# Kernel optimization log

Hardware: AMD Instinct MI355X
Metric: run time of the kernel (lower is better)

The kernel has to match this reference:

```python
import jax, jax.numpy as jnp
import numpy as np

GROUP = 128  # W4A16 quantization group size along the input (reduction) dim


def dequant(q, s, z):
    """Dequantize int4 weights. q: [out, in] ints in [0,16); s, z: [out, in//GROUP]."""
    out_f, in_f = q.shape
    g = in_f // GROUP
    qf = q.reshape(out_f, g, GROUP).astype(s.dtype)
    w = (qf - z[:, :, None]) * s[:, :, None]
    return w.reshape(out_f, in_f)


def setup_inputs() -> dict:
    key = jax.random.key(0)
    ks = jax.random.split(key, 11)
    H, I = 4096, 11008
    B, S = 4, 2048
    x = jax.random.normal(ks[0], (B, S, H), dtype=jnp.float32)
    qw_gate = jax.random.randint(ks[1], (I, H), 0, 16, dtype=jnp.int32)
    qw_up = jax.random.randint(ks[2], (I, H), 0, 16, dtype=jnp.int32)
    qw_down = jax.random.randint(ks[3], (H, I), 0, 16, dtype=jnp.int32)
    # scales small so dequantized weights have realistic magnitude; zeros in [0,16)
    s_gate = jax.random.uniform(ks[4], (I, H // GROUP), dtype=jnp.float32) * 0.01
    z_gate = jax.random.uniform(ks[5], (I, H // GROUP), dtype=jnp.float32) * 16.0
    s_up = jax.random.uniform(ks[6], (I, H // GROUP), dtype=jnp.float32) * 0.01
    z_up = jax.random.uniform(ks[7], (I, H // GROUP), dtype=jnp.float32) * 16.0
    s_down = jax.random.uniform(ks[8], (H, I // GROUP), dtype=jnp.float32) * 0.01
    z_down = jax.random.uniform(ks[9], (H, I // GROUP), dtype=jnp.float32) * 16.0
    return {
        "x": x,
        "qw_gate": qw_gate, "qw_up": qw_up, "qw_down": qw_down,
        "s_gate": s_gate, "z_gate": z_gate,
        "s_up": s_up, "z_up": z_up,
        "s_down": s_down, "z_down": z_down,
    }


def reference(x, qw_gate, qw_up, qw_down, s_gate, z_gate, s_up, z_up, s_down, z_down):
    # W4A16 SwiGLU MLP: down( silu(gate(x)) * up(x) )
    Wg = dequant(qw_gate, s_gate, z_gate)   # [I, H]
    Wu = dequant(qw_up, s_up, z_up)         # [I, H]
    Wd = dequant(qw_down, s_down, z_down)   # [H, I]
    g = jnp.einsum('bsh,ih->bsi', x, Wg)
    u = jnp.einsum('bsh,ih->bsi', x, Wu)
    h = jax.nn.silu(g) * u
    return jnp.einsum('bsi,hi->bsh', h, Wd)
```

## Files before the change

kernel.cpp:

```cpp
#include <hip/hip_runtime.h>
#include <hip/hip_fp16.h>

typedef __attribute__((ext_vector_type(8))) short s16x8;
typedef __attribute__((ext_vector_type(8))) _Float16 f16x8;
typedef __attribute__((ext_vector_type(4))) float f32x4;

__global__ void cvt_f32_to_f16_kernel(const float* __restrict__ in,
                                      __half* __restrict__ out, long n) {
  long i = (long)blockIdx.x * blockDim.x + threadIdx.x;
  long stride = (long)gridDim.x * blockDim.x;
  const float4* p4 = (const float4*)in;
  for (long j = i; j * 8 < n; j += stride) {
    float4 a = p4[j * 2];
    float4 b = p4[j * 2 + 1];
    union { s16x8 v; __half2 h2[4]; } w;
    w.h2[0] = __floats2half2_rn(a.x, a.y);
    w.h2[1] = __floats2half2_rn(a.z, a.w);
    w.h2[2] = __floats2half2_rn(b.x, b.y);
    w.h2[3] = __floats2half2_rn(b.z, b.w);
    *(s16x8*)(out + j * 8) = w.v;
  }
}

__global__ void pack_kernel(const int* __restrict__ q, uint32_t* __restrict__ p,
                            long n8) {
  long i = (long)blockIdx.x * blockDim.x + threadIdx.x;
  long stride = (long)gridDim.x * blockDim.x;
  for (; i < n8; i += stride) {
    int4 a = ((const int4*)q)[2 * i];
    int4 b = ((const int4*)q)[2 * i + 1];
    uint32_t w = (uint32_t)a.x | ((uint32_t)a.y << 4) | ((uint32_t)a.z << 8) |
                 ((uint32_t)a.w << 12) | ((uint32_t)b.x << 16) |
                 ((uint32_t)b.y << 20) | ((uint32_t)b.z << 24) |
                 ((uint32_t)b.w << 28);
    p[i] = w;
  }
}

__device__ __forceinline__ s16x8 dq_compute(int4 q0, int4 q1, float s, float z) {
  __half hs = __float2half(s);
  __half2 s2 = __halves2half2(hs, hs);
  __half hc = __float2half(-(64.f + z) * s);
  __half2 c2 = __halves2half2(hc, hc);
  uint32_t b0 = 0x54005400u + ((uint32_t)q0.x << 4) + ((uint32_t)q0.y << 20);
  uint32_t b1 = 0x54005400u + ((uint32_t)q0.z << 4) + ((uint32_t)q0.w << 20);
  uint32_t b2 = 0x54005400u + ((uint32_t)q1.x << 4) + ((uint32_t)q1.y << 20);
  uint32_t b3 = 0x54005400u + ((uint32_t)q1.z << 4) + ((uint32_t)q1.w << 20);
  union { s16x8 v; __half2 h2[4]; } w;
  w.h2[0] = __hfma2(*(__half2*)&b0, s2, c2);
  w.h2[1] = __hfma2(*(__half2*)&b1, s2, c2);
  w.h2[2] = __hfma2(*(__half2*)&b2, s2, c2);
  w.h2[3] = __hfma2(*(__half2*)&b3, s2, c2);
  return w.v;
}

__device__ __forceinline__ s16x8 dq8(uint32_t w, __half2 s2, __half2 c2) {
  union { s16x8 v; __half2 h2[4]; } r;
#pragma unroll
  for (int i = 0; i < 4; ++i) {
    uint32_t t = (w >> (8 * i)) & 0xFFu;
    uint32_t b = 0x54005400u + ((t & 15u) << 4) + ((t >> 4) << 20);
    r.h2[i] = __hfma2(*(__half2*)&b, s2, c2);
  }
  return r.v;
}

__device__ __forceinline__ int xcd_swz(int w0, int nwg) {
  const int q = nwg >> 3, r = nwg & 7;
  const int xcd = w0 & 7, idx = w0 >> 3;
  const int base = (xcd < r) ? xcd * (q + 1) : r * (q + 1) + (xcd - r) * q;
  return base + idx;
}

template <int EPI, int PK>
__global__ __launch_bounds__(512, 2)
void qgemm_x_kernel(const __half* __restrict__ Xh,
                    const int* __restrict__ Q, const uint32_t* __restrict__ QP,
                    const float* __restrict__ S, const float* __restrict__ Z,
                    __half* __restrict__ Pan, int mbs) {
  constexpr int H = 4096, I = 11008, G = 32;
  const int wg = xcd_swz(blockIdx.x, gridDim.x);
  const int mb = wg % mbs;
  const int nb = wg / mbs;
  const int m0 = mb * 256;
  const int n0 = nb * 128;
  const int tid = threadIdx.x;
  const int lane = tid & 63;
  const int wave = tid >> 6;
  const int wm = (wave >> 1) * 64, wn = (wave & 1) * 64;
  const int l15 = lane & 15, lq = lane >> 4;
  const int rsw = (l15 & 7) << 3;

  __shared__ __half As[2][256][64];
  __shared__ __half Bs[2][128][64];

  f32x4 acc[4][4];
#pragma unroll
  for (int i = 0; i < 4; ++i)
#pragma unroll
    for (int j = 0; j < 4; ++j) acc[i][j] = {0.f, 0.f, 0.f, 0.f};

  const int arowD = tid >> 3;
  const int acolD = (((tid & 7) ^ ((tid >> 3) & 7)) << 3);
  const int qrow = tid >> 2, qcol0 = (tid & 3) * 16, qsw = (qrow & 7) << 3;
  const int*      qP  = Q  + (size_t)(n0 + qrow) * H + qcol0;
  const uint32_t* qPp = QP + (size_t)(n0 + qrow) * (H / 8) + (tid & 3) * 2;
  const float* sP = S + (size_t)(n0 + qrow) * G;
  const float* zP = Z + (size_t)(n0 + qrow) * G;

  int4 qA[4], qB[4];
  uint32_t wA0, wA1, wB0, wB1;
  float sA, zA, sB, zB;

#define STAGE_A(buf, kk)                                              \
  {                                                                   \
    const int _k = (kk);                                              \
    _Pragma("unroll")                                                 \
    for (int c = 0; c < 4; ++c) {                                     \
      const __half* src = Xh + (size_t)(m0 + c * 64 + arowD) * H + _k + acolD; \
      __half* dst = &As[buf][0][0] + (size_t)(c * 512 + tid) * 8;     \
      __builtin_amdgcn_global_load_lds((const __attribute__((address_space(1))) void*)src, \
                                       (__attribute__((address_space(3))) void*)dst, 16, 0, 0); \
    }                                                                 \
  }
#define LOAD_Q(set, kk)                                               \
  {                                                                   \
    const int _k = (kk);                                              \
    if (PK) {                                                         \
      w##set##0 = qPp[_k >> 3]; w##set##1 = qPp[(_k >> 3) + 1];       \
    } else {                                                          \
      _Pragma("unroll")                                               \
      for (int i = 0; i < 4; ++i) q##set[i] = ((const int4*)(qP + _k))[i]; \
    }                                                                 \
    s##set = sP[_k >> 7]; z##set = zP[_k >> 7];                       \
  }
#define WRITE_B(buf, set)                                             \
  {                                                                   \
    if (PK) {                                                         \
      __half hs = __float2half(s##set);                               \
      __half2 s2 = __halves2half2(hs, hs);                            \
      __half hc = __float2half(-(64.f + z##set) * s##set);            \
      __half2 c2 = __halves2half2(hc, hc);                            \
      *(s16x8*)&Bs[buf][qrow][(qcol0 + 0) ^ qsw] = dq8(w##set##0, s2, c2); \
      *(s16x8*)&Bs[buf][qrow][(qcol0 + 8) ^ qsw] = dq8(w##set##1, s2, c2); \
    } else {                                                          \
      *(s16x8*)&Bs[buf][qrow][(qcol0 + 0) ^ qsw] = dq_compute(q##set[0], q##set[1], s##set, z##set); \
      *(s16x8*)&Bs[buf][qrow][(qcol0 + 8) ^ qsw] = dq_compute(q##set[2], q##set[3], s##set, z##set); \
    }                                                                 \
  }
#define MFMA_BUF(buf)                                                 \
  {                                                                   \
    __builtin_amdgcn_s_setprio(1);                                    \
    _Pragma("unroll")                                                 \
    for (int kk = 0; kk < 2; ++kk) {                                  \
      const int cbase = (kk * 32 + lq * 8) ^ rsw;                     \
      f16x8 af[4];                                                    \
      _Pragma("unroll")                                               \
      for (int i = 0; i < 4; ++i)                                     \
        af[i] = *(const f16x8*)&As[buf][wm + i * 16 + l15][cbase];    \
      _Pragma("unroll")                                               \
      for (int j = 0; j < 4; ++j) {                                   \
        f16x8 bf = *(const f16x8*)&Bs[buf][wn + j * 16 + l15][cbase]; \
        _Pragma("unroll")                                             \
        for (int i = 0; i < 4; ++i)                                   \
          acc[i][j] = __builtin_amdgcn_mfma_f32_16x16x32_f16(af[i], bf, acc[i][j], 0, 0, 0); \
      }                                                               \
    }                                                                 \
    __builtin_amdgcn_s_setprio(0);                                    \
  }

  const int nt = H / 64;
  STAGE_A(0, 0)
  LOAD_Q(A, 0)
  LOAD_Q(B, 64)
  WRITE_B(0, A)
  __syncthreads();

  for (int t = 0; t < nt; t += 2) {
    if (t + 1 < nt) STAGE_A(1, (t + 1) * 64)
    if (t + 2 < nt) LOAD_Q(A, (t + 2) * 64)
    MFMA_BUF(0)
    if (t + 1 < nt) WRITE_B(1, B)
    __syncthreads();
    if (t + 2 < nt) STAGE_A(0, (t + 2) * 64)
    if (t + 3 < nt) LOAD_Q(B, (t + 3) * 64)
    MFMA_BUF(1)
    if (t + 2 < nt) WRITE_B(0, A)
    __syncthreads();
  }
#undef STAGE_A
#undef LOAD_Q
#undef WRITE_B
#undef MFMA_BUF

#pragma unroll
  for (int i = 0; i < 4; ++i)
#pragma unroll
    for (int j = 0; j < 4; ++j)
#pragma unroll
      for (int r = 0; r < 4; ++r) {
        const int row = m0 + wm + i * 16 + lq * 4 + r;
        const int col = n0 + wn + j * 16 + l15;
        const size_t idx = (size_t)row * I + col;
        if (EPI == 0) {
          Pan[idx] = __float2half(acc[i][j][r]);
        } else {
          float g = __half2float(Pan[idx]);
          float u = acc[i][j][r];
          Pan[idx] = __float2half((g / (1.f + __expf(-g))) * u);
        }
      }
}

template <int PK>
__global__ __launch_bounds__(512, 2)
void down_kernel(const __half* __restrict__ Hws,
                 const int* __restrict__ Qd, const uint32_t* __restrict__ QdP,
                 const float* __restrict__ Sd, const float* __restrict__ Zd,
                 float* __restrict__ Out, int mbs) {
  constexpr int K = 11008, N = 4096, G = 86;
  const int wg = xcd_swz(blockIdx.x, gridDim.x);
  const int mb = wg % mbs;
  const int nb = wg / mbs;
  const int m0 = mb * 256, n0 = nb * 128;
  const int tid = threadIdx.x;
  const int lane = tid & 63;
  const int wave = tid >> 6;
  const int wm = (wave >> 1) * 64, wn = (wave & 1) * 64;
  const int l15 = lane & 15, lq = lane >> 4;
  const int rsw = (l15 & 7) << 3;

  __shared__ __half As[2][256][64];
  __shared__ __half Bs[2][128][64];

  f32x4 acc[4][4];
#pragma unroll
  for (int i = 0; i < 4; ++i)
#pragma unroll
    for (int j = 0; j < 4; ++j) acc[i][j] = {0.f, 0.f, 0.f, 0.f};

  const int arowD = tid >> 3;
  const int acolD = (((tid & 7) ^ ((tid >> 3) & 7)) << 3);
  const int qrow = tid >> 2, qcol0 = (tid & 3) * 16, qsw = (qrow & 7) << 3;
  const int*      qP  = Qd  + (size_t)(n0 + qrow) * K + qcol0;
  const uint32_t* qPp = QdP + (size_t)(n0 + qrow) * (K / 8) + (tid & 3) * 2;
  const float* sP = Sd + (size_t)(n0 + qrow) * G;
  const float* zP = Zd + (size_t)(n0 + qrow) * G;

  int4 qA[4], qB[4];
  uint32_t wA0, wA1, wB0, wB1;
  float sA, zA, sB, zB;

#define STAGE_A(buf, kk)                                              \
  {                                                                   \
    const int _k = (kk);                                              \
    _Pragma("unroll")                                                 \
    for (int c = 0; c < 4; ++c) {                                     \
      const __half* src = Hws + (size_t)(m0 + c * 64 + arowD) * K + _k + acolD; \
      __half* dst = &As[buf][0][0] + (size_t)(c * 512 + tid) * 8;     \
      __builtin_amdgcn_global_load_lds((const __attribute__((address_space(1))) void*)src, \
                                       (__attribute__((address_space(3))) void*)dst, 16, 0, 0); \
    }                                                                 \
  }
#define LOAD_Q(set, kk)                                               \
  {                                                                   \
    const int _k = (kk);                                              \
    if (PK) {                                                         \
      w##set##0 = qPp[_k >> 3]; w##set##1 = qPp[(_k >> 3) + 1];       \
    } else {                                                          \
      _Pragma("unroll")                                               \
      for (int i = 0; i < 4; ++i) q##set[i] = ((const int4*)(qP + _k))[i]; \
    }                                                                 \
    s##set = sP[_k >> 7]; z##set = zP[_k >> 7];                       \
  }
#define WRITE_B(buf, set)                                             \
  {                                                                   \
    if (PK) {                                                         \
      __half hs = __float2half(s##set);                               \
      __half2 s2 = __halves2half2(hs, hs);                            \
      __half hc = __float2half(-(64.f + z##set) * s##set);            \
      __half2 c2 = __halves2half2(hc, hc);                            \
      *(s16x8*)&Bs[buf][qrow][(qcol0 + 0) ^ qsw] = dq8(w##set##0, s2, c2); \
      *(s16x8*)&Bs[buf][qrow][(qcol0 + 8) ^ qsw] = dq8(w##set##1, s2, c2); \
    } else {                                                          \
      *(s16x8*)&Bs[buf][qrow][(qcol0 + 0) ^ qsw] = dq_compute(q##set[0], q##set[1], s##set, z##set); \
      *(s16x8*)&Bs[buf][qrow][(qcol0 + 8) ^ qsw] = dq_compute(q##set[2], q##set[3], s##set, z##set); \
    }                                                                 \
  }
#define MFMA_BUF(buf)                                                 \
  {                                                                   \
    __builtin_amdgcn_s_setprio(1);                                    \
    _Pragma("unroll")                                                 \
    for (int kk = 0; kk < 2; ++kk) {                                  \
      const int cbase = (kk * 32 + lq * 8) ^ rsw;                     \
      f16x8 af[4];                                                    \
      _Pragma("unroll")                                               \
      for (int i = 0; i < 4; ++i)                                     \
        af[i] = *(const f16x8*)&As[buf][wm + i * 16 + l15][cbase];    \
      _Pragma("unroll")                                               \
      for (int j = 0; j < 4; ++j) {                                   \
        f16x8 bf = *(const f16x8*)&Bs[buf][wn + j * 16 + l15][cbase]; \
        _Pragma("unroll")                                             \
        for (int i = 0; i < 4; ++i)                                   \
          acc[i][j] = __builtin_amdgcn_mfma_f32_16x16x32_f16(af[i], bf, acc[i][j], 0, 0, 0); \
      }                                                               \
    }                                                                 \
    __builtin_amdgcn_s_setprio(0);                                    \
  }

  const int nt = K / 64;
  STAGE_A(0, 0)
  LOAD_Q(A, 0)
  LOAD_Q(B, 64)
  WRITE_B(0, A)
  __syncthreads();

  for (int t = 0; t < nt; t += 2) {
    if (t + 1 < nt) STAGE_A(1, (t + 1) * 64)
    if (t + 2 < nt) LOAD_Q(A, (t + 2) * 64)
    MFMA_BUF(0)
    if (t + 1 < nt) WRITE_B(1, B)
    __syncthreads();
    if (t + 2 < nt) STAGE_A(0, (t + 2) * 64)
    if (t + 3 < nt) LOAD_Q(B, (t + 3) * 64)
    MFMA_BUF(1)
    if (t + 2 < nt) WRITE_B(0, A)
    __syncthreads();
  }
#undef STAGE_A
#undef LOAD_Q
#undef WRITE_B
#undef MFMA_BUF

#pragma unroll
  for (int i = 0; i < 4; ++i)
#pragma unroll
    for (int j = 0; j < 4; ++j)
#pragma unroll
      for (int r = 0; r < 4; ++r) {
        const int row = m0 + wm + i * 16 + lq * 4 + r;
        const int col = n0 + wn + j * 16 + l15;
        Out[(size_t)row * N + col] = acc[i][j][r];
      }
}

extern "C" void kernel_launch(void* const* d_in, const int* in_sizes, int n_in,
                              void* d_out, int out_size, void* d_ws, size_t ws_size,
                              hipStream_t stream) {
  const float* x  = (const float*)d_in[0];
  const int* qg   = (const int*)d_in[1];
  const int* qu   = (const int*)d_in[2];
  const int* qd   = (const int*)d_in[3];
  const float* sg = (const float*)d_in[4];
  const float* zg = (const float*)d_in[5];
  const float* su = (const float*)d_in[6];
  const float* zu = (const float*)d_in[7];
  const float* sd = (const float*)d_in[8];
  const float* zd = (const float*)d_in[9];
  float* out = (float*)d_out;

  const int M = 8192, H = 4096, I = 11008;
  const long N8 = (long)I * H / 8;

  const int PD_MAX = 1375, PU_MAX = 2751, PG_MAX = 4127;
  uint32_t* Pd = (uint32_t*)d_out;
  uint32_t* Pu = Pd + N8;
  uint32_t* Pg = Pu + N8;

  pack_kernel<<<2048, 256, 0, stream>>>(qd, Pd, N8);
  pack_kernel<<<2048, 256, 0, stream>>>(qu, Pu, N8);
  pack_kernel<<<2048, 256, 0, stream>>>(qg, Pg, N8);

  const size_t per_row = (size_t)(H + I) * 2;
  long mc = (long)(ws_size / per_row);
  mc &= ~255L;
  if (mc > M) mc = M;
  if (mc < 256) mc = 256;
  const int nch = (int)((M + mc - 1) / mc);
  int base = ((M / nch) / 256) * 256;
  if (base < 256) base = 256;
  int rem = M - base * nch;
  const int nplus = rem > 0 ? rem / 256 : 0;

  __half* wsx = (__half*)d_ws;
  const int McMax = base + (nplus > 0 ? 256 : 0);
  __half* wsh = (__half*)((char*)d_ws + (size_t)McMax * H * 2);

  int mbs_arr[64], mb_arr[64];
  {
    int mb = 0;
    for (int c = 0; c < nch; ++c) {
      int r = base + (c < nplus ? 256 : 0);
      mb_arr[c] = mb;
      mbs_arr[c] = r / 256;
      mb += r;
    }
  }

  int W = M;
  for (int c = nch - 1; c >= 0; --c) {
    const int mbase = mb_arr[c];
    const int mbs = mbs_arr[c];
    const int rows = mbs * 256;
    const bool g_pk = (PG_MAX < W);
    const bool u_pk = (PU_MAX < W);
    const bool d_pk = (PD_MAX < mbase);

    cvt_f32_to_f16_kernel<<<1024, 256, 0, stream>>>(
        x + (size_t)mbase * H, wsx, (long)rows * H);

    if (g_pk)
      qgemm_x_kernel<0, 1><<<mbs * (I / 128), 512, 0, stream>>>(
          wsx, qg, Pg, sg, zg, wsh, mbs);
    else
      qgemm_x_kernel<0, 0><<<mbs * (I / 128), 512, 0, stream>>>(
          wsx, qg, Pg, sg, zg, wsh, mbs);

    if (u_pk)
      qgemm_x_kernel<1, 1><<<mbs * (I / 128), 512, 0, stream>>>(
          wsx, qu, Pu, su, zu, wsh, mbs);
    else
      qgemm_x_kernel<1, 0><<<mbs * (I / 128), 512, 0, stream>>>(
          wsx, qu, Pu, su, zu, wsh, mbs);

    if (d_pk)
      down_kernel<1><<<mbs * (H / 128), 512, 0, stream>>>(
          wsh, qd, Pd, sd, zd, out + (size_t)mbase * H, mbs);
    else
      down_kernel<0><<<mbs * (H / 128), 512, 0, stream>>>(
          wsh, qd, Pd, sd, zd, out + (size_t)mbase * H, mbs);

    W = mbase;
  }
}
```

Measured before the change: 3.750 ms.

## Fuse gate and up projections into one kernel with dual accumulators

The separate gate and up GEMM kernels are merged into one gateup kernel that stages each X tile once and multiplies it against both dequantized weight tiles, keeping two accumulator sets and applying SiLU(g)*u in the epilogue. This removes the second read of the fp16 activations and the write-then-read round trip of the gate result through the workspace. In exchange, register pressure doubles (32 f32x4 accumulators) and LDS use grows, which may cut occupancy below the two-blocks-per-CU target. The packed-weight placement in the output buffer and the pack/no-pack thresholds are reordered to fit the fused layout.

```diff
diff --git a/kernel.cpp b/kernel.cpp
--- a/kernel.cpp
+++ b/kernel.cpp
@@ -72,12 +72,14 @@
   return base + idx;
 }
 
-template <int EPI, int PK>
+template <int PK>
 __global__ __launch_bounds__(512, 2)
-void qgemm_x_kernel(const __half* __restrict__ Xh,
-                    const int* __restrict__ Q, const uint32_t* __restrict__ QP,
-                    const float* __restrict__ S, const float* __restrict__ Z,
-                    __half* __restrict__ Pan, int mbs) {
+void gateup_kernel(const __half* __restrict__ Xh,
+                   const int* __restrict__ Qg, const uint32_t* __restrict__ Pg,
+                   const int* __restrict__ Qu, const uint32_t* __restrict__ Pu,
+                   const float* __restrict__ Sg, const float* __restrict__ Zg,
+                   const float* __restrict__ Su, const float* __restrict__ Zu,
+                   __half* __restrict__ Pan, int mbs) {
   constexpr int H = 4096, I = 11008, G = 32;
   const int wg = xcd_swz(blockIdx.x, gridDim.x);
   const int mb = wg % mbs;
@@ -92,25 +94,33 @@
   const int rsw = (l15 & 7) << 3;
 
   __shared__ __half As[2][256][64];
-  __shared__ __half Bs[2][128][64];
-
-  f32x4 acc[4][4];
+  __shared__ __half Bg[2][128][64];
+  __shared__ __half Bu[2][128][64];
+
+  f32x4 accg[4][4], accu[4][4];
 #pragma unroll
   for (int i = 0; i < 4; ++i)
 #pragma unroll
-    for (int j = 0; j < 4; ++j) acc[i][j] = {0.f, 0.f, 0.f, 0.f};
+    for (int j = 0; j < 4; ++j) {
+      accg[i][j] = {0.f, 0.f, 0.f, 0.f};
+      accu[i][j] = {0.f, 0.f, 0.f, 0.f};
+    }
 
   const int arowD = tid >> 3;
   const int acolD = (((tid & 7) ^ ((tid >> 3) & 7)) << 3);
   const int qrow = tid >> 2, qcol0 = (tid & 3) * 16, qsw = (qrow & 7) << 3;
-  const int*      qP  = Q  + (size_t)(n0 + qrow) * H + qcol0;
-  const uint32_t* qPp = QP + (size_t)(n0 + qrow) * (H / 8) + (tid & 3) * 2;
-  const float* sP = S + (size_t)(n0 + qrow) * G;
-  const float* zP = Z + (size_t)(n0 + qrow) * G;
-
-  int4 qA[4], qB[4];
-  uint32_t wA0, wA1, wB0, wB1;
-  float sA, zA, sB, zB;
+  const int*      qPg = Qg + (size_t)(n0 + qrow) * H + qcol0;
+  const int*      qPu = Qu + (size_t)(n0 + qrow) * H + qcol0;
+  const uint32_t* pPg = Pg + (size_t)(n0 + qrow) * (H / 8) + (tid & 3) * 2;
+  const uint32_t* pPu = Pu + (size_t)(n0 + qrow) * (H / 8) + (tid & 3) * 2;
+  const float* sPg = Sg + (size_t)(n0 + qrow) * G;
+  const float* zPg = Zg + (size_t)(n0 + qrow) * G;
+  const float* sPu = Su + (size_t)(n0 + qrow) * G;
+  const float* zPu = Zu + (size_t)(n0 + qrow) * G;
+
+  int4 qG[4], qU[4];
+  uint32_t wG0, wG1, wU0, wU1;
+  float sG, zG, sU, zU;
 
 #define STAGE_A(buf, kk)                                              \
   {                                                                   \
@@ -123,29 +133,41 @@
                                        (__attribute__((address_space(3))) void*)dst, 16, 0, 0); \
     }                                                                 \
   }
-#define LOAD_Q(set, kk)                                               \
+#define LOAD_Q(kk)                                                    \
   {                                                                   \
     const int _k = (kk);                                              \
     if (PK) {                                                         \
-      w##set##0 = qPp[_k >> 3]; w##set##1 = qPp[(_k >> 3) + 1];       \
+      wG0 = pPg[_k >> 3]; wG1 = pPg[(_k >> 3) + 1];                   \
+      wU0 = pPu[_k >> 3]; wU1 = pPu[(_k >> 3) + 1];                   \
     } else {                                                          \
       _Pragma("unroll")                                               \
-      for (int i = 0; i < 4; ++i) q##set[i] = ((const int4*)(qP + _k))[i]; \
-    }                                                                 \
-    s##set = sP[_k >> 7]; z##set = zP[_k >> 7];                       \
-  }
-#define WRITE_B(buf, set)                                             \
+      for (int i = 0; i < 4; ++i) qG[i] = ((const int4*)(qPg + _k))[i]; \
+      _Pragma("unroll")                                               \
+      for (int i = 0; i < 4; ++i) qU[i] = ((const int4*)(qPu + _k))[i]; \
+    }                                                                 \
+    sG = sPg[_k >> 7]; zG = zPg[_k >> 7];                             \
+    sU = sPu[_k >> 7]; zU = zPu[_k >> 7];                             \
+  }
+#define WRITE_B(buf)                                                  \
   {                                                                   \
     if (PK) {                                                         \
-      __half hs = __float2half(s##set);                               \
-      __half2 s2 = __halves2half2(hs, hs);                            \
-      __half hc = __float2half(-(64.f + z##set) * s##set);            \
-      __half2 c2 = __halves2half2(hc, hc);                            \
-      *(s16x8*)&Bs[buf][qrow][(qcol0 + 0) ^ qsw] = dq8(w##set##0, s2, c2); \
-      *(s16x8*)&Bs[buf][qrow][(qcol0 + 8) ^ qsw] = dq8(w##set##1, s2, c2); \
+      __half h1 = __float2half(sG);                                   \
+      __half2 s2 = __halves2half2(h1, h1);                            \
+      __half h2 = __float2half(-(64.f + zG) * sG);                    \
+      __half2 c2 = __halves2half2(h2, h2);                            \
+      *(s16x8*)&Bg[buf][qrow][(qcol0 + 0) ^ qsw] = dq8(wG0, s2, c2);  \
+      *(s16x8*)&Bg[buf][qrow][(qcol0 + 8) ^ qsw] = dq8(wG1, s2, c2);  \
+      __half h3 = __float2half(sU);                                   \
+      __half2 s3 = __halves2half2(h3, h3);                            \
+      __half h4 = __float2half(-(64.f + zU) * sU);                    \
+      __half2 c3 = __halves2half2(h4, h4);                            \
+      *(s16x8*)&Bu[buf][qrow][(qcol0 + 0) ^ qsw] = dq8(wU0, s3, c3);  \
+      *(s16x8*)&Bu[buf][qrow][(qcol0 + 8) ^ qsw] = dq8(wU1, s3, c3);  \
     } else {                                                          \
-      *(s16x8*)&Bs[buf][qrow][(qcol0 + 0) ^ qsw] = dq_compute(q##set[0], q##set[1], s##set, z##set); \
-      *(s16x8*)&Bs[buf][qrow][(qcol0 + 8) ^ qsw] = dq_compute(q##set[2], q##set[3], s##set, z##set); \
+      *(s16x8*)&Bg[buf][qrow][(qcol0 + 0) ^ qsw] = dq_compute(qG[0], qG[1], sG, zG); \
+      *(s16x8*)&Bg[buf][qrow][(qcol0 + 8) ^ qsw] = dq_compute(qG[2], qG[3], sG, zG); \
+      *(s16x8*)&Bu[buf][qrow][(qcol0 + 0) ^ qsw] = dq_compute(qU[0], qU[1], sU, zU); \
+      *(s16x8*)&Bu[buf][qrow][(qcol0 + 8) ^ qsw] = dq_compute(qU[2], qU[3], sU, zU); \
     }                                                                 \
   }
 #define MFMA_BUF(buf)                                                 \
@@ -160,10 +182,13 @@
         af[i] = *(const f16x8*)&As[buf][wm + i * 16 + l15][cbase];    \
       _Pragma("unroll")                                               \
       for (int j = 0; j < 4; ++j) {                                   \
-        f16x8 bf = *(const f16x8*)&Bs[buf][wn + j * 16 + l15][cbase]; \
+        f16x8 bg = *(const f16x8*)&Bg[buf][wn + j * 16 + l15][cbase]; \
+        f16x8 bu = *(const f16x8*)&Bu[buf][wn + j * 16 + l15][cbase]; \
         _Pragma("unroll")                                             \
-        for (int i = 0; i < 4; ++i)                                   \
-          acc[i][j] = __builtin_amdgcn_mfma_f32_16x16x32_f16(af[i], bf, acc[i][j], 0, 0, 0); \
+        for (int i = 0; i < 4; ++i) {                                 \
+          accg[i][j] = __builtin_amdgcn_mfma_f32_16x16x32_f16(af[i], bg, accg[i][j], 0, 0, 0); \
+          accu[i][j] = __builtin_amdgcn_mfma_f32_16x16x32_f16(af[i], bu, accu[i][j], 0, 0, 0); \
+        }                                                             \
       }                                                               \
     }                                                                 \
     __builtin_amdgcn_s_setprio(0);                                    \
@@ -171,22 +196,20 @@
 
   const int nt = H / 64;
   STAGE_A(0, 0)
-  LOAD_Q(A, 0)
-  LOAD_Q(B, 64)
-  WRITE_B(0, A)
+  LOAD_Q(0)
+  WRITE_B(0)
   __syncthreads();
 
-  for (int t = 0; t < nt; t += 2) {
-    if (t + 1 < nt) STAGE_A(1, (t + 1) * 64)
-    if (t + 2 < nt) LOAD_Q(A, (t + 2) * 64)
-    MFMA_BUF(0)
-    if (t + 1 < nt) WRITE_B(1, B)
+  int p = 0;
+  for (int t = 0; t < nt; ++t) {
+    if (t + 1 < nt) {
+      STAGE_A(p ^ 1, (t + 1) * 64)
+      LOAD_Q((t + 1) * 64)
+    }
+    MFMA_BUF(p)
+    if (t + 1 < nt) WRITE_B(p ^ 1)
     __syncthreads();
-    if (t + 2 < nt) STAGE_A(0, (t + 2) * 64)
-    if (t + 3 < nt) LOAD_Q(B, (t + 3) * 64)
-    MFMA_BUF(1)
-    if (t + 2 < nt) WRITE_B(0, A)
-    __syncthreads();
+    p ^= 1;
   }
 #undef STAGE_A
 #undef LOAD_Q
@@ -201,14 +224,10 @@
       for (int r = 0; r < 4; ++r) {
         const int row = m0 + wm + i * 16 + lq * 4 + r;
         const int col = n0 + wn + j * 16 + l15;
-        const size_t idx = (size_t)row * I + col;
-        if (EPI == 0) {
-          Pan[idx] = __float2half(acc[i][j][r]);
-        } else {
-          float g = __half2float(Pan[idx]);
-          float u = acc[i][j][r];
-          Pan[idx] = __float2half((g / (1.f + __expf(-g))) * u);
-        }
+        float g = accg[i][j][r];
+        float u = accu[i][j][r];
+        float hv = (g / (1.f + __expf(-g))) * u;
+        Pan[(size_t)row * I + col] = __float2half(hv);
       }
 }
 
@@ -362,14 +381,14 @@
   const int M = 8192, H = 4096, I = 11008;
   const long N8 = (long)I * H / 8;
 
-  const int PD_MAX = 1375, PU_MAX = 2751, PG_MAX = 4127;
+  const int PD_MAX = 1375, PU_MAX = 4127;
   uint32_t* Pd = (uint32_t*)d_out;
-  uint32_t* Pu = Pd + N8;
-  uint32_t* Pg = Pu + N8;
+  uint32_t* Pg = Pd + N8;
+  uint32_t* Pu = Pg + N8;
 
   pack_kernel<<<2048, 256, 0, stream>>>(qd, Pd, N8);
+  pack_kernel<<<2048, 256, 0, stream>>>(qg, Pg, N8);
   pack_kernel<<<2048, 256, 0, stream>>>(qu, Pu, N8);
-  pack_kernel<<<2048, 256, 0, stream>>>(qg, Pg, N8);
 
   const size_t per_row = (size_t)(H + I) * 2;
   long mc = (long)(ws_size / per_row);
@@ -402,26 +421,18 @@
     const int mbase = mb_arr[c];
     const int mbs = mbs_arr[c];
     const int rows = mbs * 256;
-    const bool g_pk = (PG_MAX < W);
-    const bool u_pk = (PU_MAX < W);
-    const bool d_pk = (PD_MAX < mbase);
+    const bool gu_pk = (PU_MAX < W);
+    const bool d_pk = (PD_MAX < W) && (PD_MAX < mbase);
 
     cvt_f32_to_f16_kernel<<<1024, 256, 0, stream>>>(
         x + (size_t)mbase * H, wsx, (long)rows * H);
 
-    if (g_pk)
-      qgemm_x_kernel<0, 1><<<mbs * (I / 128), 512, 0, stream>>>(
-          wsx, qg, Pg, sg, zg, wsh, mbs);
+    if (gu_pk)
+      gateup_kernel<1><<<mbs * (I / 128), 512, 0, stream>>>(
+          wsx, qg, Pg, qu, Pu, sg, zg, su, zu, wsh, mbs);
     else
-      qgemm_x_kernel<0, 0><<<mbs * (I / 128), 512, 0, stream>>>(
-          wsx, qg, Pg, sg, zg, wsh, mbs);
-
-    if (u_pk)
-      qgemm_x_kernel<1, 1><<<mbs * (I / 128), 512, 0, stream>>>(
-          wsx, qu, Pu, su, zu, wsh, mbs);
-    else
-      qgemm_x_kernel<1, 0><<<mbs * (I / 128), 512, 0, stream>>>(
-          wsx, qu, Pu, su, zu, wsh, mbs);
+      gateup_kernel<0><<<mbs * (I / 128), 512, 0, stream>>>(
+          wsx, qg, Pg, qu, Pu, sg, zg, su, zu, wsh, mbs);
 
     if (d_pk)
       down_kernel<1><<<mbs * (H / 128), 512, 0, stream>>>(
```

New measurement: 3.383 ms. 9.8% less time.
